# Kernel tuning notes

Hardware: AMD Instinct MI355X
Metric: run time of the kernel (lower is better)

The kernel has to match this reference:

```python
import jax, jax.numpy as jnp
import numpy as np

HIDDEN = 768
HEADS = 12
HEAD_DIM = HIDDEN // HEADS
LN_EPS = 1e-12


def setup_inputs() -> dict:
    key = jax.random.key(0)
    ks = jax.random.split(key, 12)
    B, Lq, Lk = 8, 512, 1024
    s = 0.02
    return {
        "query": jax.random.normal(ks[0], (B, Lq, HIDDEN), jnp.float32),
        "key": jax.random.normal(ks[1], (B, Lk, HIDDEN), jnp.float32),
        "value": jax.random.normal(ks[2], (B, Lk, HIDDEN), jnp.float32),
        "attention_mask": jnp.zeros((B, 1, 1, Lk), jnp.float32),
        "q_attention_mask": jnp.zeros((B, 1, 1, Lq), jnp.float32),
        "Wq": jax.random.normal(ks[3], (HIDDEN, HIDDEN), jnp.float32) * s,
        "bq": jnp.zeros((HIDDEN,), jnp.float32),
        "Wk": jax.random.normal(ks[4], (HIDDEN, HIDDEN), jnp.float32) * s,
        "bk": jnp.zeros((HIDDEN,), jnp.float32),
        "Wv": jax.random.normal(ks[5], (HIDDEN, HIDDEN), jnp.float32) * s,
        "bv": jnp.zeros((HIDDEN,), jnp.float32),
        "Wo": jax.random.normal(ks[6], (HIDDEN, HIDDEN), jnp.float32) * s,
        "bo": jnp.zeros((HIDDEN,), jnp.float32),
        "ln_gamma": jnp.ones((HIDDEN,), jnp.float32),
        "ln_beta": jnp.zeros((HIDDEN,), jnp.float32),
    }


def _split_heads(x):  # [B, L, H*D] -> [B, H, L, D]
    B, L, _ = x.shape
    return x.reshape(B, L, HEADS, HEAD_DIM).transpose(0, 2, 1, 3)


def reference(query, key, value, attention_mask, q_attention_mask,
              Wq, bq, Wk, bk, Wv, bv, Wo, bo, ln_gamma, ln_beta):
    # QKV projections (dropout is identity at inference)
    q = _split_heads(query @ Wq.T + bq)   # [B,H,Lq,D]
    k = _split_heads(key @ Wk.T + bk)     # [B,H,Lk,D]
    v = _split_heads(value @ Wv.T + bv)   # [B,H,Lk,D]

    scores = jnp.einsum("bhqd,bhkd->bhqk", q, k) / jnp.sqrt(
        jnp.asarray(HEAD_DIM, q.dtype))
    scores = scores + attention_mask  # additive mask broadcast [B,1,1,Lk]
    probs = jax.nn.softmax(scores, axis=-1)
    ctx = jnp.einsum("bhqk,bhkd->bhqd", probs, v)  # [B,H,Lq,D]
    B, H, Lq, D = ctx.shape
    ctx = ctx.transpose(0, 2, 1, 3).reshape(B, Lq, H * D)

    # BertSelfOutput: dense + residual + LayerNorm
    h = ctx @ Wo.T + bo + query
    mu = jnp.mean(h, axis=-1, keepdims=True)
    var = jnp.mean(jnp.square(h - mu), axis=-1, keepdims=True)
    out = (h - mu) / jnp.sqrt(var + LN_EPS) * ln_gamma + ln_beta
    return out, probs
```

## Files before the change

### kernel.cpp

```cpp
#include <hip/hip_runtime.h>
#include <math.h>

#define HIDDEN 768
#define NHEADS 12
#define DHEAD  64
#define NB     8
#define LQ     512
#define LK     1024
#define LN_EPS 1e-12f
#define STRIDE_S 1028

typedef __attribute__((ext_vector_type(8))) short short8;
typedef __attribute__((ext_vector_type(4))) float floatx4;

#define GLDS16(gp, lp) __builtin_amdgcn_global_load_lds( \
    (const __attribute__((address_space(1))) void*)(gp), \
    (__attribute__((address_space(3))) void*)(lp), 16, 0, 0)

__device__ __forceinline__ short f2bf(float f) {
    unsigned u = __float_as_uint(f);
    u = u + 0x7FFFu + ((u >> 16) & 1u);
    return (short)(u >> 16);
}

__global__ __launch_bounds__(256)
void cvt_f32_bf16(const float* __restrict__ in, short* __restrict__ out, int n4)
{
    int i = blockIdx.x * 256 + threadIdx.x;
    if (i >= n4) return;
    float4 v = ((const float4*)in)[i];
    short4 o;
    o.x = f2bf(v.x); o.y = f2bf(v.y); o.z = f2bf(v.z); o.w = f2bf(v.w);
    ((short4*)out)[i] = o;
}

__global__ __launch_bounds__(256)
void gemm_nt_mfma(const short* __restrict__ A, const short* __restrict__ B,
                  float* __restrict__ Cf, short* __restrict__ Cb,
                  const float* __restrict__ bias, const float* __restrict__ res,
                  int K, int lda, int ldb, int ldc, float alpha)
{
    __shared__ short As[4096];
    __shared__ short Bs[4096];

    int n0 = blockIdx.x * 128;
    int m0 = blockIdx.y * 128;
    int t    = threadIdx.x;
    int lane = t & 63, wave = t >> 6;
    int quad = lane >> 4, l15 = lane & 15;
    int wr = wave >> 1, wc = wave & 1;

    int e0 = t, e1 = 256 + t;
    int r0 = e0 >> 2, c0 = (e0 & 3) ^ ((r0 >> 1) & 3);
    int r1 = e1 >> 2, c1 = (e1 & 3) ^ ((r1 >> 1) & 3);
    const short* Ap0 = A + (size_t)(m0 + r0) * lda + c0 * 8;
    const short* Ap1 = A + (size_t)(m0 + r1) * lda + c1 * 8;
    const short* Bp0 = B + (size_t)(n0 + r0) * ldb + c0 * 8;
    const short* Bp1 = B + (size_t)(n0 + r1) * ldb + c1 * 8;

    int aoff[4], boff[4];
#pragma unroll
    for (int i = 0; i < 4; i++) {
        int ra = wr * 64 + i * 16 + l15;
        aoff[i] = (ra * 4 + (quad ^ ((ra >> 1) & 3))) * 8;
        int rb = wc * 64 + i * 16 + l15;
        boff[i] = (rb * 4 + (quad ^ ((rb >> 1) & 3))) * 8;
    }

    floatx4 acc[4][4] = {};

    for (int k0 = 0; k0 < K; k0 += 32) {
        GLDS16(Ap0, &As[e0 * 8]);
        GLDS16(Ap1, &As[e1 * 8]);
        GLDS16(Bp0, &Bs[e0 * 8]);
        GLDS16(Bp1, &Bs[e1 * 8]);
        Ap0 += 32; Ap1 += 32; Bp0 += 32; Bp1 += 32;
        __syncthreads();

        short8 af[4], bfr[4];
#pragma unroll
        for (int i = 0; i < 4; i++) af[i]  = *(const short8*)&As[aoff[i]];
#pragma unroll
        for (int j = 0; j < 4; j++) bfr[j] = *(const short8*)&Bs[boff[j]];
#pragma unroll
        for (int i = 0; i < 4; i++)
#pragma unroll
            for (int j = 0; j < 4; j++)
                acc[i][j] = __builtin_amdgcn_mfma_f32_16x16x32_bf16(
                    af[i], bfr[j], acc[i][j], 0, 0, 0);
        __syncthreads();
    }

#pragma unroll
    for (int i = 0; i < 4; i++) {
        int mb = m0 + wr * 64 + i * 16 + quad * 4;
#pragma unroll
        for (int j = 0; j < 4; j++) {
            int n = n0 + wc * 64 + j * 16 + l15;
            float bv = bias ? bias[n] : 0.f;
#pragma unroll
            for (int r = 0; r < 4; r++) {
                int m = mb + r;
                float v = alpha * acc[i][j][r] + bv;
                if (res) v += res[(size_t)m * ldc + n];
                if (Cb) Cb[(size_t)m * ldc + n] = f2bf(v);
                else    Cf[(size_t)m * ldc + n] = v;
            }
        }
    }
}

__global__ __launch_bounds__(256)
void transpose_v(const short* __restrict__ vb, short* __restrict__ vt)
{
    __shared__ short T[256 * 72];
    int kt = blockIdx.x, bh = blockIdx.y;
    int b = bh / 12, h = bh - b * 12;
    int t = threadIdx.x;
    const short* src = vb + ((size_t)b * LK + kt * 256) * HIDDEN + h * DHEAD;
#pragma unroll
    for (int it = 0; it < 8; it++) {
        int s = it * 256 + t;
        int k = s >> 3, c = s & 7;
        *(short8*)&T[k * 72 + c * 8] =
            *(const short8*)&src[(size_t)k * HIDDEN + c * 8];
    }
    __syncthreads();
    short* dst = vt + (size_t)bh * DHEAD * LK + kt * 256;
#pragma unroll
    for (int it = 0; it < 8; it++) {
        int s = it * 256 + t;
        int d = s >> 5, kc = s & 31;
        short8 v;
#pragma unroll
        for (int i = 0; i < 8; i++) v[i] = T[(kc * 8 + i) * 72 + d];
        *(short8*)&dst[(size_t)d * LK + kc * 8] = v;
    }
}

__global__ __launch_bounds__(256)
void fused_attn(const short* __restrict__ qb, const short* __restrict__ kb,
                const short* __restrict__ vt, const float* __restrict__ amask,
                float* __restrict__ probs, short* __restrict__ ctxb)
{
    __shared__ float S[32 * STRIDE_S];
    __shared__ short KV[8192];
    __shared__ short Qs[2048];
    __shared__ float maskL[1024];
    __shared__ float mpart[4][32];
    __shared__ float mrow[32], lrow[32];

    int qt = blockIdx.x;
    int bh = blockIdx.y;
    int b  = bh / 12, h = bh - b * 12;
    int m0 = qt * 32;

    const short* Qg = qb + ((size_t)b * LQ + m0) * HIDDEN + h * DHEAD;
    const short* Kg = kb + (size_t)b * LK * HIDDEN + h * DHEAD;
    const short* Vg = vt + (size_t)bh * DHEAD * LK;
    const float* Mg = amask + (size_t)b * LK;
    float* Pg = probs + (size_t)bh * LQ * LK + (size_t)m0 * LK;
    short* Cg = ctxb + ((size_t)b * LQ + m0) * HIDDEN + h * DHEAD;

    int t = threadIdx.x;
    int lane = t & 63, w = t >> 6;
    int quad = lane >> 4, l15 = lane & 15;

    {
        int r = t >> 3, cs = t & 7, c = cs ^ (r & 7);
        GLDS16(Qg + (size_t)r * HIDDEN + c * 8, &Qs[t * 8]);
    }
    ((float4*)maskL)[t] = ((const float4*)Mg)[t];
#pragma unroll
    for (int I = 0; I < 4; I++) {
        int s = I * 256 + t;
        int r = s >> 3, cs = s & 7, c = cs ^ (r & 7);
        GLDS16(Kg + (size_t)r * HIDDEN + c * 8, &KV[s * 8]);
    }
    __syncthreads();

    short8 af[2][2];
#pragma unroll
    for (int i = 0; i < 2; i++)
#pragma unroll
        for (int ks = 0; ks < 2; ks++) {
            int row = i * 16 + l15;
            int cs = (ks * 4 + quad) ^ (row & 7);
            af[i][ks] = *(const short8*)&Qs[(row * 8 + cs) * 8];
        }

    float mx[8];
#pragma unroll
    for (int i = 0; i < 8; i++) mx[i] = -3.0e38f;

    for (int kc = 0; kc < 8; kc++) {
        floatx4 acc[2][2] = {};
#pragma unroll
        for (int ks = 0; ks < 2; ks++)
#pragma unroll
            for (int j = 0; j < 2; j++) {
                int rK = w * 32 + j * 16 + l15;
                int cs = (ks * 4 + quad) ^ (rK & 7);
                short8 bf = *(const short8*)&KV[(rK * 8 + cs) * 8];
#pragma unroll
                for (int i = 0; i < 2; i++)
                    acc[i][j] = __builtin_amdgcn_mfma_f32_16x16x32_bf16(
                        af[i][ks], bf, acc[i][j], 0, 0, 0);
            }
        __syncthreads();
        if (kc < 7) {
            const short* Kn = Kg + (size_t)(kc + 1) * 128 * HIDDEN;
#pragma unroll
            for (int I = 0; I < 4; I++) {
                int s = I * 256 + t;
                int r = s >> 3, cs = s & 7, c = cs ^ (r & 7);
                GLDS16(Kn + (size_t)r * HIDDEN + c * 8, &KV[s * 8]);
            }
        }
#pragma unroll
        for (int i = 0; i < 2; i++)
#pragma unroll
            for (int j = 0; j < 2; j++) {
                int n = kc * 128 + w * 32 + j * 16 + l15;
                float mk = maskL[n];
#pragma unroll
                for (int r = 0; r < 4; r++) {
                    int m = i * 16 + quad * 4 + r;
                    float v = acc[i][j][r] * 0.125f + mk;
                    S[m * STRIDE_S + n] = v;
                    mx[i * 4 + r] = fmaxf(mx[i * 4 + r], v);
                }
            }
        __syncthreads();
    }

#pragma unroll
    for (int d = 1; d < 16; d <<= 1)
#pragma unroll
        for (int i = 0; i < 8; i++)
            mx[i] = fmaxf(mx[i], __shfl_xor(mx[i], d));
    if (l15 == 0)
#pragma unroll
        for (int i = 0; i < 2; i++)
#pragma unroll
            for (int r = 0; r < 4; r++)
                mpart[w][i * 16 + quad * 4 + r] = mx[i * 4 + r];
    __syncthreads();
    if (t < 32)
        mrow[t] = fmaxf(fmaxf(mpart[0][t], mpart[1][t]),
                        fmaxf(mpart[2][t], mpart[3][t]));
#pragma unroll
    for (int I = 0; I < 4; I++) {
        int s = I * 256 + t;
        int n = s >> 4, cs = s & 15, c = cs ^ (n & 15);
        GLDS16(Vg + (size_t)n * LK + c * 8, &KV[s * 8]);
    }
    __syncthreads();

    {
        int r = t >> 3, seg = t & 7;
        float mr = mrow[r];
        float sum = 0.f;
        float4* Srow = (float4*)&S[r * STRIDE_S + seg * 128];
#pragma unroll
        for (int i = 0; i < 32; i++) {
            float4 v = Srow[i];
            v.x = __expf(v.x - mr); v.y = __expf(v.y - mr);
            v.z = __expf(v.z - mr); v.w = __expf(v.w - mr);
            Srow[i] = v;
            sum += v.x + v.y + v.z + v.w;
        }
#pragma unroll
        for (int d = 1; d < 8; d <<= 1) sum += __shfl_xor(sum, d);
        if (seg == 0) lrow[r] = sum;
    }
    __syncthreads();

    for (int it = 0; it < 32; it++) {
        int idx = it * 256 + t;
        int r = idx >> 8, c4 = idx & 255;
        float inv = 1.0f / lrow[r];
        float4 v = *(const float4*)&S[r * STRIDE_S + c4 * 4];
        v.x *= inv; v.y *= inv; v.z *= inv; v.w *= inv;
        ((float4*)(Pg + (size_t)r * LK))[c4] = v;
    }

    int wr = w >> 1, wc = w & 1;
    floatx4 accO[2] = {};

    for (int kc = 0; kc < 8; kc++) {
        short8 pa[4];
#pragma unroll
        for (int ks = 0; ks < 4; ks++) {
            const float* sp =
                &S[(wr * 16 + l15) * STRIDE_S + kc * 128 + ks * 32 + quad * 8];
            float4 v0 = *(const float4*)sp;
            float4 v1 = *(const float4*)(sp + 4);
            short8 s8;
            s8[0]=f2bf(v0.x); s8[1]=f2bf(v0.y); s8[2]=f2bf(v0.z); s8[3]=f2bf(v0.w);
            s8[4]=f2bf(v1.x); s8[5]=f2bf(v1.y); s8[6]=f2bf(v1.z); s8[7]=f2bf(v1.w);
            pa[ks] = s8;
        }
#pragma unroll
        for (int ks = 0; ks < 4; ks++)
#pragma unroll
            for (int j = 0; j < 2; j++) {
                int n = wc * 32 + j * 16 + l15;
                int cs = (ks * 4 + quad) ^ (n & 15);
                short8 bf = *(const short8*)&KV[(n * 16 + cs) * 8];
                accO[j] = __builtin_amdgcn_mfma_f32_16x16x32_bf16(
                    pa[ks], bf, accO[j], 0, 0, 0);
            }
        __syncthreads();
        if (kc < 7) {
            const short* Vn = Vg + (kc + 1) * 128;
#pragma unroll
            for (int I = 0; I < 4; I++) {
                int s = I * 256 + t;
                int n = s >> 4, cs = s & 15, c = cs ^ (n & 15);
                GLDS16(Vn + (size_t)n * LK + c * 8, &KV[s * 8]);
            }
        }
        __syncthreads();
    }

    float inv[4];
#pragma unroll
    for (int r = 0; r < 4; r++) inv[r] = 1.0f / lrow[wr * 16 + quad * 4 + r];
#pragma unroll
    for (int j = 0; j < 2; j++) {
        int n = wc * 32 + j * 16 + l15;
#pragma unroll
        for (int r = 0; r < 4; r++) {
            int m = wr * 16 + quad * 4 + r;
            Cg[(size_t)m * HIDDEN + n] = f2bf(accO[j][r] * inv[r]);
        }
    }
}

__global__ __launch_bounds__(256)
void layernorm_rows(const float* __restrict__ H, const float* __restrict__ gamma,
                    const float* __restrict__ beta, float* __restrict__ out)
{
    int row = blockIdx.x;
    const float* h = H + (long)row * HIDDEN;
    int t = threadIdx.x;

    float x[3];
    float s = 0.f, ss = 0.f;
#pragma unroll
    for (int i = 0; i < 3; i++) {
        x[i] = h[t + 256 * i];
        s  += x[i];
        ss += x[i] * x[i];
    }
#pragma unroll
    for (int off = 32; off > 0; off >>= 1) {
        s  += __shfl_down(s, off);
        ss += __shfl_down(ss, off);
    }
    __shared__ float sh_s[4], sh_ss[4];
    int wave = t >> 6;
    if ((t & 63) == 0) { sh_s[wave] = s; sh_ss[wave] = ss; }
    __syncthreads();
    float S  = sh_s[0] + sh_s[1] + sh_s[2] + sh_s[3];
    float SS = sh_ss[0] + sh_ss[1] + sh_ss[2] + sh_ss[3];

    float mu  = S * (1.0f / HIDDEN);
    float var = SS * (1.0f / HIDDEN) - mu * mu;
    float inv = rsqrtf(var + LN_EPS);

    float* o = out + (long)row * HIDDEN;
#pragma unroll
    for (int i = 0; i < 3; i++) {
        int c = t + 256 * i;
        o[c] = (x[i] - mu) * inv * gamma[c] + beta[c];
    }
}

extern "C" void kernel_launch(void* const* d_in, const int* in_sizes, int n_in,
                              void* d_out, int out_size, void* d_ws, size_t ws_size,
                              hipStream_t stream)
{
    const float* query = (const float*)d_in[0];
    const float* key   = (const float*)d_in[1];
    const float* value = (const float*)d_in[2];
    const float* amask = (const float*)d_in[3];
    const float* Wq    = (const float*)d_in[5];
    const float* bq    = (const float*)d_in[6];
    const float* Wk    = (const float*)d_in[7];
    const float* bk    = (const float*)d_in[8];
    const float* Wv    = (const float*)d_in[9];
    const float* bv    = (const float*)d_in[10];
    const float* Wo    = (const float*)d_in[11];
    const float* bo    = (const float*)d_in[12];
    const float* gamma = (const float*)d_in[13];
    const float* beta  = (const float*)d_in[14];

    short* qx = (short*)d_ws;
    short* kx = qx + (long)4096 * 768;
    short* vx = kx + (long)8192 * 768;
    short* wq = vx + (long)8192 * 768;
    short* wk = wq + (long)768 * 768;
    short* wv = wk + (long)768 * 768;
    short* wo = wv + (long)768 * 768;
    short* qb = wo + (long)768 * 768;
    short* kb = qb + (long)4096 * 768;
    short* vb = kb + (long)8192 * 768;
    short* ctxb = qx;
    short* vt   = kx;
    float* hbuf = (float*)vx;

    float* out0  = (float*)d_out;
    float* probs = out0 + (long)NB * LQ * HIDDEN;

    cvt_f32_bf16<<<(4096 * 768 / 4 + 255) / 256, 256, 0, stream>>>(query, qx, 4096 * 768 / 4);
    cvt_f32_bf16<<<(8192 * 768 / 4 + 255) / 256, 256, 0, stream>>>(key,   kx, 8192 * 768 / 4);
    cvt_f32_bf16<<<(8192 * 768 / 4 + 255) / 256, 256, 0, stream>>>(value, vx, 8192 * 768 / 4);
    cvt_f32_bf16<<<(768 * 768 / 4 + 255) / 256, 256, 0, stream>>>(Wq, wq, 768 * 768 / 4);
    cvt_f32_bf16<<<(768 * 768 / 4 + 255) / 256, 256, 0, stream>>>(Wk, wk, 768 * 768 / 4);
    cvt_f32_bf16<<<(768 * 768 / 4 + 255) / 256, 256, 0, stream>>>(Wv, wv, 768 * 768 / 4);
    cvt_f32_bf16<<<(768 * 768 / 4 + 255) / 256, 256, 0, stream>>>(Wo, wo, 768 * 768 / 4);

    gemm_nt_mfma<<<dim3(6, 32), 256, 0, stream>>>(
        qx, wq, nullptr, qb, bq, nullptr, HIDDEN, HIDDEN, HIDDEN, HIDDEN, 1.0f);
    gemm_nt_mfma<<<dim3(6, 64), 256, 0, stream>>>(
        kx, wk, nullptr, kb, bk, nullptr, HIDDEN, HIDDEN, HIDDEN, HIDDEN, 1.0f);
    gemm_nt_mfma<<<dim3(6, 64), 256, 0, stream>>>(
        vx, wv, nullptr, vb, bv, nullptr, HIDDEN, HIDDEN, HIDDEN, HIDDEN, 1.0f);

    transpose_v<<<dim3(4, 96), 256, 0, stream>>>(vb, vt);

    fused_attn<<<dim3(16, 96), 256, 0, stream>>>(qb, kb, vt, amask, probs, ctxb);

    gemm_nt_mfma<<<dim3(6, 32), 256, 0, stream>>>(
        ctxb, wo, hbuf, nullptr, bo, query, HIDDEN, HIDDEN, HIDDEN, HIDDEN, 1.0f);

    layernorm_rows<<<NB * LQ, 256, 0, stream>>>(hbuf, gamma, beta, out0);
}
```

Before: 544.7 us.

## Store attention scores as bf16 in LDS and read K/V directly from global

```diff
diff --git a/kernel.cpp b/kernel.cpp
--- a/kernel.cpp
+++ b/kernel.cpp
@@ -8,7 +8,7 @@
 #define LQ     512
 #define LK     1024
 #define LN_EPS 1e-12f
-#define STRIDE_S 1028
+#define TS     1032
 
 typedef __attribute__((ext_vector_type(8))) short short8;
 typedef __attribute__((ext_vector_type(4))) float floatx4;
@@ -21,6 +21,10 @@
     unsigned u = __float_as_uint(f);
     u = u + 0x7FFFu + ((u >> 16) & 1u);
     return (short)(u >> 16);
+}
+
+__device__ __forceinline__ float bf2f(short s) {
+    return __uint_as_float(((unsigned)(unsigned short)s) << 16);
 }
 
 __global__ __launch_bounds__(256)
@@ -143,16 +147,15 @@
                 const short* __restrict__ vt, const float* __restrict__ amask,
                 float* __restrict__ probs, short* __restrict__ ctxb)
 {
-    __shared__ float S[32 * STRIDE_S];
-    __shared__ short KV[8192];
-    __shared__ short Qs[2048];
-    __shared__ float maskL[1024];
+    __shared__ short S[32 * TS];
     __shared__ float mpart[4][32];
     __shared__ float mrow[32], lrow[32];
 
-    int qt = blockIdx.x;
-    int bh = blockIdx.y;
-    int b  = bh / 12, h = bh - b * 12;
+    int flat = blockIdx.y * 16 + blockIdx.x;
+    int jj   = flat >> 3;
+    int bh   = (flat & 7) * 12 + jj % 12;
+    int qt   = jj / 12;
+    int b = bh / 12, h = bh - b * 12;
     int m0 = qt * 32;
 
     const short* Qg = qb + ((size_t)b * LQ + m0) * HIDDEN + h * DHEAD;
@@ -166,72 +169,41 @@
     int lane = t & 63, w = t >> 6;
     int quad = lane >> 4, l15 = lane & 15;
 
-    {
-        int r = t >> 3, cs = t & 7, c = cs ^ (r & 7);
-        GLDS16(Qg + (size_t)r * HIDDEN + c * 8, &Qs[t * 8]);
-    }
-    ((float4*)maskL)[t] = ((const float4*)Mg)[t];
-#pragma unroll
-    for (int I = 0; I < 4; I++) {
-        int s = I * 256 + t;
-        int r = s >> 3, cs = s & 7, c = cs ^ (r & 7);
-        GLDS16(Kg + (size_t)r * HIDDEN + c * 8, &KV[s * 8]);
-    }
-    __syncthreads();
-
     short8 af[2][2];
 #pragma unroll
     for (int i = 0; i < 2; i++)
 #pragma unroll
+        for (int ks = 0; ks < 2; ks++)
+            af[i][ks] = *(const short8*)&Qg[(size_t)(i * 16 + l15) * HIDDEN
+                                            + ks * 32 + quad * 8];
+
+    float mx[8];
+#pragma unroll
+    for (int i = 0; i < 8; i++) mx[i] = -3.0e38f;
+
+#pragma unroll 4
+    for (int kc = 0; kc < 16; kc++) {
+        int n = kc * 64 + w * 16 + l15;
+        const short* Kp = Kg + (size_t)n * HIDDEN;
+        floatx4 acc[2] = {};
+#pragma unroll
         for (int ks = 0; ks < 2; ks++) {
-            int row = i * 16 + l15;
-            int cs = (ks * 4 + quad) ^ (row & 7);
-            af[i][ks] = *(const short8*)&Qs[(row * 8 + cs) * 8];
+            short8 bfr = *(const short8*)&Kp[ks * 32 + quad * 8];
+#pragma unroll
+            for (int i = 0; i < 2; i++)
+                acc[i] = __builtin_amdgcn_mfma_f32_16x16x32_bf16(
+                    af[i][ks], bfr, acc[i], 0, 0, 0);
         }
-
-    float mx[8];
-#pragma unroll
-    for (int i = 0; i < 8; i++) mx[i] = -3.0e38f;
-
-    for (int kc = 0; kc < 8; kc++) {
-        floatx4 acc[2][2] = {};
-#pragma unroll
-        for (int ks = 0; ks < 2; ks++)
-#pragma unroll
-            for (int j = 0; j < 2; j++) {
-                int rK = w * 32 + j * 16 + l15;
-                int cs = (ks * 4 + quad) ^ (rK & 7);
-                short8 bf = *(const short8*)&KV[(rK * 8 + cs) * 8];
-#pragma unroll
-                for (int i = 0; i < 2; i++)
-                    acc[i][j] = __builtin_amdgcn_mfma_f32_16x16x32_bf16(
-                        af[i][ks], bf, acc[i][j], 0, 0, 0);
+        float mk = Mg[n];
+#pragma unroll
+        for (int i = 0; i < 2; i++)
+#pragma unroll
+            for (int r = 0; r < 4; r++) {
+                int m = i * 16 + quad * 4 + r;
+                float v = acc[i][r] * 0.125f + mk;
+                S[m * TS + n] = f2bf(v);
+                mx[i * 4 + r] = fmaxf(mx[i * 4 + r], v);
             }
-        __syncthreads();
-        if (kc < 7) {
-            const short* Kn = Kg + (size_t)(kc + 1) * 128 * HIDDEN;
-#pragma unroll
-            for (int I = 0; I < 4; I++) {
-                int s = I * 256 + t;
-                int r = s >> 3, cs = s & 7, c = cs ^ (r & 7);
-                GLDS16(Kn + (size_t)r * HIDDEN + c * 8, &KV[s * 8]);
-            }
-        }
-#pragma unroll
-        for (int i = 0; i < 2; i++)
-#pragma unroll
-            for (int j = 0; j < 2; j++) {
-                int n = kc * 128 + w * 32 + j * 16 + l15;
-                float mk = maskL[n];
-#pragma unroll
-                for (int r = 0; r < 4; r++) {
-                    int m = i * 16 + quad * 4 + r;
-                    float v = acc[i][j][r] * 0.125f + mk;
-                    S[m * STRIDE_S + n] = v;
-                    mx[i * 4 + r] = fmaxf(mx[i * 4 + r], v);
-                }
-            }
-        __syncthreads();
     }
 
 #pragma unroll
@@ -249,79 +221,61 @@
     if (t < 32)
         mrow[t] = fmaxf(fmaxf(mpart[0][t], mpart[1][t]),
                         fmaxf(mpart[2][t], mpart[3][t]));
-#pragma unroll
-    for (int I = 0; I < 4; I++) {
-        int s = I * 256 + t;
-        int n = s >> 4, cs = s & 15, c = cs ^ (n & 15);
-        GLDS16(Vg + (size_t)n * LK + c * 8, &KV[s * 8]);
-    }
     __syncthreads();
 
     {
         int r = t >> 3, seg = t & 7;
         float mr = mrow[r];
         float sum = 0.f;
-        float4* Srow = (float4*)&S[r * STRIDE_S + seg * 128];
-#pragma unroll
-        for (int i = 0; i < 32; i++) {
-            float4 v = Srow[i];
-            v.x = __expf(v.x - mr); v.y = __expf(v.y - mr);
-            v.z = __expf(v.z - mr); v.w = __expf(v.w - mr);
-            Srow[i] = v;
-            sum += v.x + v.y + v.z + v.w;
+#pragma unroll 4
+        for (int i = 0; i < 16; i++) {
+            int u = i * 8 + seg;
+            short8 v = *(const short8*)&S[r * TS + u * 8];
+            short8 o;
+#pragma unroll
+            for (int e = 0; e < 8; e++) {
+                float f = __expf(bf2f(v[e]) - mr);
+                o[e] = f2bf(f);
+                sum += f;
+            }
+            *(short8*)&S[r * TS + u * 8] = o;
         }
-#pragma unroll
-        for (int d = 1; d < 8; d <<= 1) sum += __shfl_xor(sum, d);
+        sum += __shfl_xor(sum, 1);
+        sum += __shfl_xor(sum, 2);
+        sum += __shfl_xor(sum, 4);
         if (seg == 0) lrow[r] = sum;
     }
     __syncthreads();
 
-    for (int it = 0; it < 32; it++) {
-        int idx = it * 256 + t;
-        int r = idx >> 8, c4 = idx & 255;
+#pragma unroll 2
+    for (int r = 0; r < 32; r++) {
         float inv = 1.0f / lrow[r];
-        float4 v = *(const float4*)&S[r * STRIDE_S + c4 * 4];
-        v.x *= inv; v.y *= inv; v.z *= inv; v.w *= inv;
-        ((float4*)(Pg + (size_t)r * LK))[c4] = v;
+        short4 v = *(const short4*)&S[r * TS + t * 4];
+        float4 o;
+        o.x = bf2f(v.x) * inv; o.y = bf2f(v.y) * inv;
+        o.z = bf2f(v.z) * inv; o.w = bf2f(v.w) * inv;
+        ((float4*)(Pg + (size_t)r * LK))[t] = o;
     }
 
     int wr = w >> 1, wc = w & 1;
     floatx4 accO[2] = {};
-
-    for (int kc = 0; kc < 8; kc++) {
-        short8 pa[4];
-#pragma unroll
-        for (int ks = 0; ks < 4; ks++) {
-            const float* sp =
-                &S[(wr * 16 + l15) * STRIDE_S + kc * 128 + ks * 32 + quad * 8];
-            float4 v0 = *(const float4*)sp;
-            float4 v1 = *(const float4*)(sp + 4);
-            short8 s8;
-            s8[0]=f2bf(v0.x); s8[1]=f2bf(v0.y); s8[2]=f2bf(v0.z); s8[3]=f2bf(v0.w);
-            s8[4]=f2bf(v1.x); s8[5]=f2bf(v1.y); s8[6]=f2bf(v1.z); s8[7]=f2bf(v1.w);
-            pa[ks] = s8;
-        }
-#pragma unroll
-        for (int ks = 0; ks < 4; ks++)
+#pragma unroll 4
+    for (int kc = 0; kc < 16; kc++) {
+        short8 pa[2];
+#pragma unroll
+        for (int ks = 0; ks < 2; ks++)
+            pa[ks] = *(const short8*)&S[(wr * 16 + l15) * TS
+                                        + kc * 64 + ks * 32 + quad * 8];
+#pragma unroll
+        for (int ks = 0; ks < 2; ks++)
 #pragma unroll
             for (int j = 0; j < 2; j++) {
                 int n = wc * 32 + j * 16 + l15;
-                int cs = (ks * 4 + quad) ^ (n & 15);
-                short8 bf = *(const short8*)&KV[(n * 16 + cs) * 8];
+                short8 bfr = *(const short8*)&Vg[(size_t)n * LK
+                                                 + kc * 64 + ks * 32 + quad * 8];
                 accO[j] = __builtin_amdgcn_mfma_f32_16x16x32_bf16(
-                    pa[ks], bf, accO[j], 0, 0, 0);
+                    pa[ks], bfr, accO[j], 0, 0, 0);
             }
-        __syncthreads();
-        if (kc < 7) {
-            const short* Vn = Vg + (kc + 1) * 128;
-#pragma unroll
-            for (int I = 0; I < 4; I++) {
-                int s = I * 256 + t;
-                int n = s >> 4, cs = s & 15, c = cs ^ (n & 15);
-                GLDS16(Vn + (size_t)n * LK + c * 8, &KV[s * 8]);
-            }
-        }
-        __syncthreads();
     }
 
     float inv[4];
```

New measurement: 565.1 us. +3.7%, slower.
